# Performance work log

Measured on AMD Instinct MI355X. Metric: run time of the kernel, lower is better.

## Reference

```python
import jax, jax.numpy as jnp
import numpy as np

B, S, D, E, K = 64, 1024, 1024, 8, 2
Z_COEF = 1e-3      # router_z_loss_coef
AUX_COEF = 1e-3    # router_aux_loss_coef


def setup_inputs() -> dict:
    key = jax.random.key(0)
    k1, k2, k3 = jax.random.split(key, 3)
    x = jax.random.normal(k1, (B, S, D), dtype=jnp.float32)
    # xavier-uniform-ish init for query weight, randn for expert keys (as in torch init)
    lim_q = float(np.sqrt(6.0 / (D + D)))
    Wq = jax.random.uniform(k2, (D, D), dtype=jnp.float32, minval=-lim_q, maxval=lim_q)
    bq = jnp.zeros((D,), dtype=jnp.float32)
    lim_k = float(np.sqrt(6.0 / (E + D)))
    key_emb = jax.random.uniform(k3, (E, D), dtype=jnp.float32, minval=-lim_k, maxval=lim_k)
    return {"x": x, "Wq": Wq, "bq": bq, "key_emb": key_emb}


def reference(x, Wq, bq, key_emb):
    b, s, d = x.shape
    e = key_emb.shape[0]
    scale = d ** (-0.5)

    # q = Linear(x); attn over expert keys
    q = jnp.einsum('bsd,od->bso', x, Wq) + bq              # [B,S,D]
    attn_scores = jnp.einsum('bsd,ed->bse', q, key_emb) * scale  # [B,S,E]
    attn_weights = jax.nn.softmax(attn_scores, axis=-1)    # [B,S,E]

    # per-batch expert scores, top-k selection, scatter mask
    scores = attn_weights.mean(axis=1)                     # [B,E]
    top_k_scores, top_k_indices = jax.lax.top_k(scores, K)  # [B,K]
    mask2d = jnp.zeros_like(scores).at[jnp.arange(b)[:, None], top_k_indices].set(1.0)  # [B,E]
    mask = jnp.broadcast_to(mask2d[:, None, :], (b, s, e))  # [B,S,E]

    # routing loss: KL(load-balance) + entropy-style aux
    total_tokens = b * s
    expert_usage_prob = mask2d.sum(axis=0) * (s / total_tokens)   # == mask.sum((0,1))/total
    ideal_prob = jnp.full((e,), 1.0 / e, dtype=scores.dtype)
    # F.kl_div(log_input, target, reduction='batchmean'): sum(t*(log t - log_in))/batch(=E)
    kl = jnp.sum(ideal_prob * (jnp.log(ideal_prob) - jnp.log(expert_usage_prob))) / e
    aux = jnp.mean(attn_weights * jnp.log(attn_weights + 1e-9))
    router_loss = Z_COEF * kl + AUX_COEF * aux

    return mask, top_k_indices, router_loss
```

## Files before the change

### kernel.cpp

```cpp
#include <hip/hip_runtime.h>
#include <math.h>

#define W2OFF  0
#define B2OFF  8192
#define SCOFF  8200
#define AUXOFF 8712
#define ZTOT   513

__global__ __launch_bounds__(256) void k01_prep(const float* __restrict__ Wq,
                                                const float* __restrict__ key,
                                                const float* __restrict__ bq,
                                                float* __restrict__ ws) {
    __shared__ __attribute__((aligned(16))) float keyl[8 * 1024];
    __shared__ float part[256 * 8];
    __shared__ float part2[64];
    int tid = threadIdx.x;
    int blk = blockIdx.x;

    if (tid < 9) {
        int i = blk * 9 + tid;
        if (i < ZTOT) ws[SCOFF + i] = 0.0f;
    }

    float4* kl4 = (float4*)keyl;
    const float4* kg4 = (const float4*)key;
    #pragma unroll
    for (int k = 0; k < 8; ++k) kl4[tid + 256 * k] = kg4[tid + 256 * k];
    __syncthreads();

    int dl = tid & 15;
    int og = tid >> 4;
    int d  = blk * 16 + dl;
    float acc[8];
    #pragma unroll
    for (int e = 0; e < 8; ++e) acc[e] = 0.0f;
    for (int oo = 0; oo < 64; ++oo) {
        int o = og * 64 + oo;
        float wv = Wq[o * 1024 + d];
        #pragma unroll
        for (int e = 0; e < 8; ++e) acc[e] += keyl[e * 1024 + o] * wv;
    }
    #pragma unroll
    for (int e = 0; e < 8; ++e) part[tid * 8 + e] = acc[e];
    __syncthreads();
    if (tid < 128) {
        int dl2 = tid >> 3, e = tid & 7;
        float s = 0.0f;
        #pragma unroll
        for (int g = 0; g < 16; ++g) s += part[(g * 16 + dl2) * 8 + e];
        ws[W2OFF + e * 1024 + blk * 16 + dl2] = s;
    }

    if (blk == 0) {
        __syncthreads();
        float p[8];
        #pragma unroll
        for (int e = 0; e < 8; ++e) p[e] = 0.0f;
        #pragma unroll
        for (int k = 0; k < 4; ++k) {
            int d2 = tid + 256 * k;
            float bv = bq[d2];
            #pragma unroll
            for (int e = 0; e < 8; ++e) p[e] += bv * keyl[e * 1024 + d2];
        }
        #pragma unroll
        for (int e = 0; e < 8; ++e) part[tid * 8 + e] = p[e];
        __syncthreads();
        if (tid < 64) {
            int e = tid & 7, g = tid >> 3;
            float s = 0.0f;
            #pragma unroll
            for (int k = 0; k < 32; ++k) s += part[(g * 32 + k) * 8 + e];
            part2[g * 8 + e] = s;
        }
        __syncthreads();
        if (tid < 8) {
            float s = 0.0f;
            #pragma unroll
            for (int g = 0; g < 8; ++g) s += part2[g * 8 + tid];
            ws[B2OFF + tid] = s;
        }
    }
}

__global__ __launch_bounds__(256) void k2_main(const float* __restrict__ x,
                                               float* __restrict__ ws) {
    __shared__ __attribute__((aligned(16))) float w2l[8 * 1024];
    __shared__ __attribute__((aligned(16))) float part[4 * 64 * 8];
    __shared__ __attribute__((aligned(16))) float sraw[64 * 8];

    int tid  = threadIdx.x;
    int blk  = blockIdx.x;
    int lane = tid & 63;
    int w    = tid >> 6;
    int batch = blk >> 4;
    int tb    = blk * 64;
    int e = lane >> 3;
    int r = lane & 7;

    float4* wl4 = (float4*)w2l;
    const float4* wg4 = (const float4*)(ws + W2OFF);
    #pragma unroll
    for (int k = 0; k < 8; ++k) wl4[tid + 256 * k] = wg4[tid + 256 * k];
    __syncthreads();

    const float4* x4 = (const float4*)x;
    float* pw = part + w * 512;

    for (int p = 0; p < 4; ++p) {
        int lt0 = w * 16 + p * 4;
        int t0  = tb + lt0;
        float acc[4][8];
        #pragma unroll
        for (int j = 0; j < 4; ++j)
            #pragma unroll
            for (int c = 0; c < 8; ++c) acc[j][c] = 0.0f;

        #pragma unroll
        for (int i = 0; i < 4; ++i) {
            float4 xr[4];
            #pragma unroll
            for (int j = 0; j < 4; ++j)
                xr[j] = x4[(size_t)(t0 + j) * 256 + i * 64 + lane];
            #pragma unroll
            for (int c = 0; c < 8; ++c) {
                float4 w4 = wl4[c * 256 + i * 64 + lane];
                #pragma unroll
                for (int j = 0; j < 4; ++j)
                    acc[j][c] += w4.x * xr[j].x + w4.y * xr[j].y +
                                 w4.z * xr[j].z + w4.w * xr[j].w;
            }
        }

        #pragma unroll
        for (int j = 0; j < 4; ++j) {
            #pragma unroll
            for (int c = 0; c < 8; ++c)
                pw[c * 64 + (lane ^ (c << 3))] = acc[j][c];
            float s = 0.0f;
            #pragma unroll
            for (int m = 0; m < 8; ++m)
                s += pw[e * 64 + ((r + 8 * m) ^ (e << 3))];
            s += __shfl_xor(s, 1);
            s += __shfl_xor(s, 2);
            s += __shfl_xor(s, 4);
            if (r == 0) sraw[(lt0 + j) * 8 + e] = s;
        }
    }
    __syncthreads();

    if (tid < 64) {
        int t = tid;
        float sv[8];
        #pragma unroll
        for (int k = 0; k < 8; ++k) {
            int c = (t + k) & 7;
            sv[c] = sraw[t * 8 + c];
        }
        const float scale = 0.03125f;
        #pragma unroll
        for (int c = 0; c < 8; ++c) sv[c] = (sv[c] + ws[B2OFF + c]) * scale;
        float mx = sv[0];
        #pragma unroll
        for (int c = 1; c < 8; ++c) mx = fmaxf(mx, sv[c]);
        float wgt[8], sm = 0.0f;
        #pragma unroll
        for (int c = 0; c < 8; ++c) { wgt[c] = expf(sv[c] - mx); sm += wgt[c]; }
        float inv = 1.0f / sm;
        float aux = 0.0f;
        #pragma unroll
        for (int c = 0; c < 8; ++c) {
            wgt[c] *= inv;
            aux += wgt[c] * logf(wgt[c] + 1e-9f);
        }
        #pragma unroll
        for (int c = 0; c < 8; ++c)
            part[c * 64 + (t ^ (c << 3))] = wgt[c];
        int e2 = t >> 3, r2 = t & 7;
        float s2 = 0.0f;
        #pragma unroll
        for (int m = 0; m < 8; ++m)
            s2 += part[e2 * 64 + ((r2 + 8 * m) ^ (e2 << 3))];
        s2 += __shfl_xor(s2, 1);
        s2 += __shfl_xor(s2, 2);
        s2 += __shfl_xor(s2, 4);
        if (r2 == 0) atomicAdd(&ws[SCOFF + batch * 8 + e2], s2);
        #pragma unroll
        for (int mk = 1; mk <= 32; mk <<= 1) aux += __shfl_xor(aux, mk);
        if (t == 0) atomicAdd(&ws[AUXOFF], aux);
    }
}

__device__ __forceinline__ void top2_of8(const float* v, int& i1, int& i2) {
    i1 = 0; float b1 = v[0];
    #pragma unroll
    for (int e = 1; e < 8; ++e) if (v[e] > b1) { b1 = v[e]; i1 = e; }
    i2 = -1; float b2 = -3.4e38f;
    #pragma unroll
    for (int e = 0; e < 8; ++e) if (e != i1 && v[e] > b2) { b2 = v[e]; i2 = e; }
}

__global__ __launch_bounds__(256) void k3_out(const float* __restrict__ ws,
                                              float* __restrict__ out) {
    int tid = threadIdx.x;
    int blk = blockIdx.x;
    int batch = blk >> 2;

    float v[8];
    #pragma unroll
    for (int e = 0; e < 8; ++e) v[e] = ws[SCOFF + batch * 8 + e];
    int i1, i2;
    top2_of8(v, i1, i2);

    float m[8];
    #pragma unroll
    for (int e = 0; e < 8; ++e) m[e] = (e == i1 || e == i2) ? 1.0f : 0.0f;
    int token = blk * 256 + tid;
    float4* o4 = (float4*)out;
    o4[token * 2]     = make_float4(m[0], m[1], m[2], m[3]);
    o4[token * 2 + 1] = make_float4(m[4], m[5], m[6], m[7]);

    if (blk == 0) {
        __shared__ int cnt[8];
        if (tid < 8) cnt[tid] = 0;
        __syncthreads();
        if (tid < 64) {
            float vv[8];
            #pragma unroll
            for (int e = 0; e < 8; ++e) vv[e] = ws[SCOFF + tid * 8 + e];
            int j1, j2;
            top2_of8(vv, j1, j2);
            out[524288 + tid * 2]     = (float)j1;
            out[524288 + tid * 2 + 1] = (float)j2;
            atomicAdd(&cnt[j1], 1);
            atomicAdd(&cnt[j2], 1);
        }
        __syncthreads();
        if (tid == 0) {
            float kl = 0.0f;
            #pragma unroll
            for (int e = 0; e < 8; ++e) {
                float usage = (float)cnt[e] / 64.0f;
                kl += 0.125f * (logf(0.125f) - logf(usage));
            }
            kl *= 0.125f;
            float aux = ws[AUXOFF] / 524288.0f;
            out[524416] = 1e-3f * kl + 1e-3f * aux;
        }
    }
}

extern "C" void kernel_launch(void* const* d_in, const int* in_sizes, int n_in,
                              void* d_out, int out_size, void* d_ws, size_t ws_size,
                              hipStream_t stream) {
    const float* x   = (const float*)d_in[0];
    const float* Wq  = (const float*)d_in[1];
    const float* bq  = (const float*)d_in[2];
    const float* key = (const float*)d_in[3];
    float* out = (float*)d_out;
    float* ws  = (float*)d_ws;

    k01_prep<<<64,   256, 0, stream>>>(Wq, key, bq, ws);
    k2_main<<<1024, 256, 0, stream>>>(x, ws);
    k3_out <<<256,  256, 0, stream>>>(ws, out);
}
```

Baseline: 382.6 us.

## Fuse output kernel into main via last-block-per-batch counters; widen prep grid

Removes the third kernel launch. The last block to finish each batch, found with an atomic counter, now writes that batch's mask and top-k indices, and a second global counter lets the final batch block compute the router loss. The prep kernel moves to 128 blocks with 8 output columns each and pads the key table in shared memory to avoid bank conflicts. This saves one launch and its dependency gap, at the cost of threadfence and atomic synchronisation and mask writes concentrated in 64 finishing blocks.

After: 497.0 us. 29.9% more time.

```diff
diff --git a/kernel.cpp b/kernel.cpp
--- a/kernel.cpp
+++ b/kernel.cpp
@@ -5,50 +5,57 @@
 #define B2OFF  8192
 #define SCOFF  8200
 #define AUXOFF 8712
-#define ZTOT   513
+#define CNTOFF 8713
+#define GDOFF  8777
+#define ZTOT   578
+#define KEYP   1088
 
 __global__ __launch_bounds__(256) void k01_prep(const float* __restrict__ Wq,
                                                 const float* __restrict__ key,
                                                 const float* __restrict__ bq,
                                                 float* __restrict__ ws) {
-    __shared__ __attribute__((aligned(16))) float keyl[8 * 1024];
+    __shared__ __attribute__((aligned(16))) float keyl[8 * KEYP];
     __shared__ float part[256 * 8];
     __shared__ float part2[64];
     int tid = threadIdx.x;
     int blk = blockIdx.x;
 
-    if (tid < 9) {
-        int i = blk * 9 + tid;
+    if (tid < 5) {
+        int i = blk * 5 + tid;
         if (i < ZTOT) ws[SCOFF + i] = 0.0f;
     }
 
-    float4* kl4 = (float4*)keyl;
-    const float4* kg4 = (const float4*)key;
-    #pragma unroll
-    for (int k = 0; k < 8; ++k) kl4[tid + 256 * k] = kg4[tid + 256 * k];
-    __syncthreads();
-
-    int dl = tid & 15;
-    int og = tid >> 4;
-    int d  = blk * 16 + dl;
+    #pragma unroll
+    for (int k = 0; k < 32; ++k) {
+        int idx = tid + 256 * k;
+        int e = idx >> 10, o = idx & 1023;
+        keyl[e * KEYP + o + (o >> 5)] = key[idx];
+    }
+    __syncthreads();
+
+    int dl = tid & 7;
+    int og = tid >> 3;
+    int d  = blk * 8 + dl;
+    int kob = og * 33;
     float acc[8];
     #pragma unroll
     for (int e = 0; e < 8; ++e) acc[e] = 0.0f;
-    for (int oo = 0; oo < 64; ++oo) {
-        int o = og * 64 + oo;
+    #pragma unroll
+    for (int oo = 0; oo < 32; ++oo) {
+        int o = og * 32 + oo;
         float wv = Wq[o * 1024 + d];
         #pragma unroll
-        for (int e = 0; e < 8; ++e) acc[e] += keyl[e * 1024 + o] * wv;
+        for (int e = 0; e < 8; ++e) acc[e] += keyl[e * KEYP + kob + oo] * wv;
     }
     #pragma unroll
     for (int e = 0; e < 8; ++e) part[tid * 8 + e] = acc[e];
     __syncthreads();
-    if (tid < 128) {
-        int dl2 = tid >> 3, e = tid & 7;
+    if (tid < 64) {
+        int d2 = tid >> 3, e = tid & 7;
         float s = 0.0f;
         #pragma unroll
-        for (int g = 0; g < 16; ++g) s += part[(g * 16 + dl2) * 8 + e];
-        ws[W2OFF + e * 1024 + blk * 16 + dl2] = s;
+        for (int g = 0; g < 32; ++g) s += part[(g * 8 + d2) * 8 + e];
+        ws[W2OFF + e * 1024 + blk * 8 + d2] = s;
     }
 
     if (blk == 0) {
@@ -60,8 +67,9 @@
         for (int k = 0; k < 4; ++k) {
             int d2 = tid + 256 * k;
             float bv = bq[d2];
-            #pragma unroll
-            for (int e = 0; e < 8; ++e) p[e] += bv * keyl[e * 1024 + d2];
+            int kd = d2 + (d2 >> 5);
+            #pragma unroll
+            for (int e = 0; e < 8; ++e) p[e] += bv * keyl[e * KEYP + kd];
         }
         #pragma unroll
         for (int e = 0; e < 8; ++e) part[tid * 8 + e] = p[e];
@@ -83,11 +91,24 @@
     }
 }
 
+__device__ __forceinline__ void top2_of8(const float* v, int& i1, int& i2) {
+    i1 = 0; float b1 = v[0];
+    #pragma unroll
+    for (int e = 1; e < 8; ++e) if (v[e] > b1) { b1 = v[e]; i1 = e; }
+    i2 = -1; float b2 = -3.4e38f;
+    #pragma unroll
+    for (int e = 0; e < 8; ++e) if (e != i1 && v[e] > b2) { b2 = v[e]; i2 = e; }
+}
+
 __global__ __launch_bounds__(256) void k2_main(const float* __restrict__ x,
-                                               float* __restrict__ ws) {
+                                               float* __restrict__ ws,
+                                               float* __restrict__ out) {
     __shared__ __attribute__((aligned(16))) float w2l[8 * 1024];
     __shared__ __attribute__((aligned(16))) float part[4 * 64 * 8];
     __shared__ __attribute__((aligned(16))) float sraw[64 * 8];
+    __shared__ float sc8[8];
+    __shared__ int cnt8[8];
+    __shared__ int s_flag;
 
     int tid  = threadIdx.x;
     int blk  = blockIdx.x;
@@ -189,63 +210,69 @@
         for (int mk = 1; mk <= 32; mk <<= 1) aux += __shfl_xor(aux, mk);
         if (t == 0) atomicAdd(&ws[AUXOFF], aux);
     }
-}
-
-__device__ __forceinline__ void top2_of8(const float* v, int& i1, int& i2) {
-    i1 = 0; float b1 = v[0];
-    #pragma unroll
-    for (int e = 1; e < 8; ++e) if (v[e] > b1) { b1 = v[e]; i1 = e; }
-    i2 = -1; float b2 = -3.4e38f;
-    #pragma unroll
-    for (int e = 0; e < 8; ++e) if (e != i1 && v[e] > b2) { b2 = v[e]; i2 = e; }
-}
-
-__global__ __launch_bounds__(256) void k3_out(const float* __restrict__ ws,
-                                              float* __restrict__ out) {
-    int tid = threadIdx.x;
-    int blk = blockIdx.x;
-    int batch = blk >> 2;
-
-    float v[8];
-    #pragma unroll
-    for (int e = 0; e < 8; ++e) v[e] = ws[SCOFF + batch * 8 + e];
-    int i1, i2;
-    top2_of8(v, i1, i2);
-
-    float m[8];
-    #pragma unroll
-    for (int e = 0; e < 8; ++e) m[e] = (e == i1 || e == i2) ? 1.0f : 0.0f;
-    int token = blk * 256 + tid;
-    float4* o4 = (float4*)out;
-    o4[token * 2]     = make_float4(m[0], m[1], m[2], m[3]);
-    o4[token * 2 + 1] = make_float4(m[4], m[5], m[6], m[7]);
-
-    if (blk == 0) {
-        __shared__ int cnt[8];
-        if (tid < 8) cnt[tid] = 0;
-        __syncthreads();
-        if (tid < 64) {
-            float vv[8];
-            #pragma unroll
-            for (int e = 0; e < 8; ++e) vv[e] = ws[SCOFF + tid * 8 + e];
-            int j1, j2;
-            top2_of8(vv, j1, j2);
-            out[524288 + tid * 2]     = (float)j1;
-            out[524288 + tid * 2 + 1] = (float)j2;
-            atomicAdd(&cnt[j1], 1);
-            atomicAdd(&cnt[j2], 1);
-        }
-        __syncthreads();
+
+    int* wsi = (int*)ws;
+    __syncthreads();
+    if (tid == 0) {
+        __threadfence();
+        int prev = atomicAdd(&wsi[CNTOFF + batch], 1);
+        s_flag = (prev == 15) ? 1 : 0;
+    }
+    __syncthreads();
+    if (s_flag) {
+        __threadfence();
+        if (tid < 8) sc8[tid] = atomicAdd(&ws[SCOFF + batch * 8 + tid], 0.0f);
+        __syncthreads();
+        float v[8];
+        #pragma unroll
+        for (int c = 0; c < 8; ++c) v[c] = sc8[c];
+        int i1, i2;
+        top2_of8(v, i1, i2);
+        float m[8];
+        #pragma unroll
+        for (int c = 0; c < 8; ++c) m[c] = (c == i1 || c == i2) ? 1.0f : 0.0f;
+        float4 mA = make_float4(m[0], m[1], m[2], m[3]);
+        float4 mB = make_float4(m[4], m[5], m[6], m[7]);
+        float4* o4 = (float4*)out;
+        int tb0 = batch << 10;
+        #pragma unroll
+        for (int t = tid; t < 1024; t += 256) {
+            o4[(size_t)(tb0 + t) * 2]     = mA;
+            o4[(size_t)(tb0 + t) * 2 + 1] = mB;
+        }
         if (tid == 0) {
-            float kl = 0.0f;
-            #pragma unroll
-            for (int e = 0; e < 8; ++e) {
-                float usage = (float)cnt[e] / 64.0f;
-                kl += 0.125f * (logf(0.125f) - logf(usage));
+            out[524288 + batch * 2]     = (float)i1;
+            out[524288 + batch * 2 + 1] = (float)i2;
+            __threadfence();
+            int p2 = atomicAdd(&wsi[GDOFF], 1);
+            s_flag = (p2 == 63) ? 2 : 0;
+        }
+        __syncthreads();
+        if (s_flag == 2) {
+            if (tid < 8) cnt8[tid] = 0;
+            __syncthreads();
+            if (tid < 64) {
+                float vv[8];
+                #pragma unroll
+                for (int c = 0; c < 8; ++c)
+                    vv[c] = atomicAdd(&ws[SCOFF + tid * 8 + c], 0.0f);
+                int j1, j2;
+                top2_of8(vv, j1, j2);
+                atomicAdd(&cnt8[j1], 1);
+                atomicAdd(&cnt8[j2], 1);
             }
-            kl *= 0.125f;
-            float aux = ws[AUXOFF] / 524288.0f;
-            out[524416] = 1e-3f * kl + 1e-3f * aux;
+            __syncthreads();
+            if (tid == 0) {
+                float kl = 0.0f;
+                #pragma unroll
+                for (int c = 0; c < 8; ++c) {
+                    float usage = (float)cnt8[c] / 64.0f;
+                    kl += 0.125f * (logf(0.125f) - logf(usage));
+                }
+                kl *= 0.125f;
+                float auxv = atomicAdd(&ws[AUXOFF], 0.0f);
+                out[524416] = 1e-3f * kl + 1e-3f * (auxv / 524288.0f);
+            }
         }
     }
 }
@@ -260,7 +287,6 @@
     float* out = (float*)d_out;
     float* ws  = (float*)d_ws;
 
-    k01_prep<<<64,   256, 0, stream>>>(Wq, key, bq, ws);
-    k2_main<<<1024, 256, 0, stream>>>(x, ws);
-    k3_out <<<256,  256, 0, stream>>>(ws, out);
-}
+    k01_prep<<<128,  256, 0, stream>>>(Wq, key, bq, ws);
+    k2_main <<<1024, 256, 0, stream>>>(x, ws, out);
+}
```
